# Kernel tuning notes

Hardware: AMD Instinct MI355X
Metric: run time of the kernel (lower is better)

## Reference

```python
import jax, jax.numpy as jnp
import numpy as np

EPS = 1e-08
NEG_WEIGHT = 0.5
B, D = 4096, 256


def setup_inputs() -> dict:
    key = jax.random.key(0)
    k1, k2 = jax.random.split(key)
    feature_a = jax.random.normal(k1, (B, D), dtype=jnp.float32)
    feature_b = jax.random.normal(k2, (B, D), dtype=jnp.float32)
    labels = jnp.ones((B,), dtype=jnp.float32)  # positive pairs on the diagonal block
    return {"feature_a": feature_a, "feature_b": feature_b, "labels": labels}


def reference(feature_a, feature_b, labels):
    b = feature_a.shape[0]
    num_neg = b - 1
    # Cosine via single GEMM instead of the torch repeat/cat loop.
    # torch.nn.CosineSimilarity: dot / max(||a||*||b||, eps)
    na = jnp.sqrt(jnp.sum(feature_a * feature_a, axis=1))  # [B]
    nb = jnp.sqrt(jnp.sum(feature_b * feature_b, axis=1))  # [B]
    dots = jnp.einsum('kd,jd->kj', feature_a, feature_b)   # [B,B] dots[k,j]=a_k.b_j
    # torch ordering: block s (shift), row k pairs a_k with b_{(k+s) % B}
    k = jnp.arange(b)
    s = jnp.arange(b)
    idx = (k[None, :] + s[:, None]) % b                    # [S,K]
    cos = dots[k[None, :], idx] / jnp.maximum(na[None, :] * nb[idx], EPS)  # [S,K]
    logits = ((cos + 1.0) * 0.5).reshape(-1)               # flatten s-major (matches torch cat order)
    labels_full = jnp.concatenate(
        [labels.reshape(-1), jnp.zeros((num_neg * b,), dtype=labels.dtype)])
    weight = jnp.concatenate(
        [jnp.ones((b,), dtype=logits.dtype),
         jnp.full((num_neg * b,), NEG_WEIGHT, dtype=logits.dtype)])
    # BCELoss(weight, reduction='sum') with torch's log clamp at -100
    log_p = jnp.maximum(jnp.log(logits), -100.0)
    log_1mp = jnp.maximum(jnp.log1p(-logits), -100.0)
    loss = -jnp.sum(weight * (labels_full * log_p + (1.0 - labels_full) * log_1mp))
    return (logits, loss)
```

## Files before the change

### kernel.cpp

```cpp
#include <hip/hip_runtime.h>
#include <stdint.h>

#define NB 4096
#define ND 256

typedef __attribute__((ext_vector_type(8))) short short8;
typedef __attribute__((ext_vector_type(4))) float f32x4;

__device__ __forceinline__ unsigned short f2bf(float f) {
    unsigned int u = __float_as_uint(f);
    u += 0x7FFFu + ((u >> 16) & 1u);
    return (unsigned short)(u >> 16);
}

__device__ __forceinline__ void gload16(const void* g, void* lds_uniform) {
    __builtin_amdgcn_global_load_lds(
        (const __attribute__((address_space(1))) void*)(uintptr_t)g,
        (__attribute__((address_space(3))) void*)(unsigned int)(uintptr_t)lds_uniform,
        16, 0, 0);
}

__global__ void __launch_bounds__(256) prep_kernel(
    const float* __restrict__ A, const float* __restrict__ Bf,
    unsigned short* __restrict__ Abf, unsigned short* __restrict__ Bbf,
    float* __restrict__ lossws)
{
    if (blockIdx.x == 0 && threadIdx.x < 64) lossws[threadIdx.x << 5] = 0.0f;
    int gw   = (blockIdx.x * 256 + threadIdx.x) >> 6;
    int lane = threadIdx.x & 63;
    const float* src; unsigned short* dst; int row;
    if (gw < NB) { src = A;  dst = Abf; row = gw; }
    else         { src = Bf; dst = Bbf; row = gw - NB; }

    float4 v = reinterpret_cast<const float4*>(src + (size_t)row * ND)[lane];
    float ss = v.x * v.x + v.y * v.y + v.z * v.z + v.w * v.w;
    #pragma unroll
    for (int off = 1; off < 64; off <<= 1) ss += __shfl_xor(ss, off);
    float rn = 1.0f / sqrtf(fmaxf(ss, 1e-30f));

    ushort4 u;
    u.x = f2bf(v.x * rn); u.y = f2bf(v.y * rn);
    u.z = f2bf(v.z * rn); u.w = f2bf(v.w * rn);
    reinterpret_cast<ushort4*>(dst + (size_t)row * ND)[lane] = u;
}

__global__ void __launch_bounds__(256, 4) gemm_kernel(
    const unsigned short* __restrict__ Abf, const unsigned short* __restrict__ Bbf,
    const float* __restrict__ labels, float* __restrict__ out,
    float* __restrict__ lossws)
{
    __shared__ __align__(16) char smem[40960];

    const int tid = threadIdx.x;
    const int w = tid >> 6, lane = tid & 63;
    const int lane15 = lane & 15, lhi = lane >> 4;
    const int bk = blockIdx.x & 31, bs = blockIdx.x >> 5;
    const int k0 = bk << 7, s0 = bs << 6;
    const int j0 = (k0 + s0) & (NB - 1);

    f32x4 acc[2][5];
    #pragma unroll
    for (int m = 0; m < 2; ++m)
        #pragma unroll
        for (int r = 0; r < 5; ++r) acc[m][r] = (f32x4)0.0f;

    auto stage = [&](int kt, char* buf) {
        #pragma unroll
        for (int i = 0; i < 2; ++i) {
            int slot0 = (i << 8) + (w << 6);
            int slot  = slot0 + lane;
            int row   = slot >> 2;
            int sch   = (slot ^ (slot >> 2) ^ (slot >> 4)) & 3;
            gload16(Abf + (size_t)(k0 + row) * ND + (kt << 5) + (sch << 3), buf + slot0 * 16);
        }
        #pragma unroll
        for (int i = 0; i < 3; ++i) {
            int slot0 = (i << 8) + (w << 6);
            int slot  = slot0 + lane;
            int row   = slot >> 2;
            int srow  = (j0 + row) & (NB - 1);
            int sch   = (slot ^ (slot >> 2) ^ (slot >> 4)) & 3;
            gload16(Bbf + (size_t)srow * ND + (kt << 5) + (sch << 3), buf + 8192 + slot0 * 16);
        }
    };

    stage(0, smem);
    __syncthreads();

    for (int kt = 0; kt < 8; ++kt) {
        char* buf = smem + ((kt & 1) ? 20480 : 0);
        if (kt < 7) stage(kt + 1, smem + ((kt & 1) ? 0 : 20480));
        const int f = (lane15 ^ (lane15 >> 2)) & 3;
        short8 a[2], b[6];
        #pragma unroll
        for (int m = 0; m < 2; ++m) {
            int row = (w << 5) + (m << 4) + lane15;
            a[m] = *reinterpret_cast<const short8*>(buf + row * 64 + ((lhi ^ f) << 4));
        }
        #pragma unroll
        for (int jf = 0; jf < 6; ++jf) {
            int row = (w << 5) + (jf << 4) + lane15;
            b[jf] = *reinterpret_cast<const short8*>(buf + 8192 + row * 64 + ((lhi ^ f) << 4));
        }
        #pragma unroll
        for (int m = 0; m < 2; ++m)
            #pragma unroll
            for (int r = 0; r < 5; ++r)
                acc[m][r] = __builtin_amdgcn_mfma_f32_16x16x32_bf16(
                    a[m], b[m + r], acc[m][r], 0, 0, 0);
        __syncthreads();
    }

    float* dw    = reinterpret_cast<float*>(smem);
    float* lpart = reinterpret_cast<float*>(smem + 32768);
    #pragma unroll
    for (int m = 0; m < 2; ++m)
        #pragma unroll
        for (int r = 0; r < 5; ++r)
            #pragma unroll
            for (int e = 0; e < 4; ++e) {
                int t = (r << 4) + lane15 - (lhi << 2) - e;
                if ((unsigned)t < 64u) {
                    int kap = (w << 5) + (m << 4) + (lhi << 2) + e;
                    dw[(t << 7) + (kap ^ (t & 31))] = acc[m][r][e];
                }
            }
    __syncthreads();

    const int t = w + (lane15 << 2);
    const int s = s0 + t;
    const int x3 = w & 3;
    const float* rowp = dw + (t << 7);
    float lacc = 0.0f;

    #pragma unroll
    for (int i = 0; i < 8; ++i) {
        int qlog  = lhi + (i << 2);
        int physq = qlog ^ (lane15 & 7);
        f32x4 d = *reinterpret_cast<const f32x4*>(rowp + (physq << 2));
        f32x4 v;
        if      (x3 == 0) { v = d; }
        else if (x3 == 1) { v[0] = d[1]; v[1] = d[0]; v[2] = d[3]; v[3] = d[2]; }
        else if (x3 == 2) { v[0] = d[2]; v[1] = d[3]; v[2] = d[0]; v[3] = d[1]; }
        else              { v[0] = d[3]; v[1] = d[2]; v[2] = d[1]; v[3] = d[0]; }

        f32x4 x, y;
        #pragma unroll
        for (int e = 0; e < 4; ++e) {
            x[e] = fmaf(v[e],  0.5f, 0.5f);
            y[e] = fmaf(v[e], -0.5f, 0.5f);
        }
        *reinterpret_cast<f32x4*>(out + (size_t)s * NB + k0 + (qlog << 2)) = x;

        float l1p0 = fmaxf(__logf(y[0]), -100.0f);
        float l1p1 = fmaxf(__logf(y[1]), -100.0f);
        float l1p2 = fmaxf(__logf(y[2]), -100.0f);
        float l1p3 = fmaxf(__logf(y[3]), -100.0f);
        if (s == 0) {
            float l1pv[4] = {l1p0, l1p1, l1p2, l1p3};
            #pragma unroll
            for (int e = 0; e < 4; ++e) {
                float lab = labels[k0 + (qlog << 2) + e];
                float lp  = fmaxf(__logf(x[e]), -100.0f);
                lacc += lab * lp + (1.0f - lab) * l1pv[e];
            }
        } else {
            lacc += 0.5f * (l1p0 + l1p1 + l1p2 + l1p3);
        }
    }

    #pragma unroll
    for (int off = 32; off > 0; off >>= 1) lacc += __shfl_down(lacc, off);
    if (lane == 0) lpart[w] = lacc;
    __syncthreads();
    if (tid == 0) {
        float tot = lpart[0] + lpart[1] + lpart[2] + lpart[3];
        atomicAdd(lossws + ((blockIdx.x & 63) << 5), -tot);
    }
}

__global__ void finalize_kernel(const float* __restrict__ lossws, float* __restrict__ out) {
    float s = 0.0f;
    for (int i = 0; i < 64; ++i) s += lossws[i << 5];
    out[(size_t)NB * NB] = s;
}

extern "C" void kernel_launch(void* const* d_in, const int* in_sizes, int n_in,
                              void* d_out, int out_size, void* d_ws, size_t ws_size,
                              hipStream_t stream) {
    (void)in_sizes; (void)n_in; (void)out_size; (void)ws_size;
    const float* A      = (const float*)d_in[0];
    const float* Bf     = (const float*)d_in[1];
    const float* labels = (const float*)d_in[2];
    float* out = (float*)d_out;

    char* ws = (char*)d_ws;
    unsigned short* Abf = (unsigned short*)ws;
    unsigned short* Bbf = (unsigned short*)(ws + (size_t)2 * 1024 * 1024);
    float* lossws = (float*)(ws + (size_t)4 * 1024 * 1024);

    hipLaunchKernelGGL(prep_kernel, dim3(2048), dim3(256), 0, stream,
                       A, Bf, Abf, Bbf, lossws);
    hipLaunchKernelGGL(gemm_kernel, dim3(2048), dim3(256), 0, stream,
                       Abf, Bbf, labels, out, lossws);
    hipLaunchKernelGGL(finalize_kernel, dim3(1), dim3(1), 0, stream, lossws, out);
}
```

Baseline: 47.33 us.

## Fold finalize into GEMM via completion counter; use explicit vmcnt waits

Drops the separate single-thread finalize kernel. The last GEMM block to finish, detected with an atomic completion counter that prep_kernel resets, sums the loss partials and writes the loss. The K-loop replaces __syncthreads with explicit s_waitcnt vmcnt plus raw s_barrier and sched barriers, so the next stage's loads stay in flight while the current tile is consumed. This removes one kernel launch and the full waits on outstanding loads, but it depends on hand-counted vmcnt values being correct for the async LDS loads.

```diff
diff --git a/kernel.cpp b/kernel.cpp
--- a/kernel.cpp
+++ b/kernel.cpp
@@ -23,9 +23,12 @@
 __global__ void __launch_bounds__(256) prep_kernel(
     const float* __restrict__ A, const float* __restrict__ Bf,
     unsigned short* __restrict__ Abf, unsigned short* __restrict__ Bbf,
-    float* __restrict__ lossws)
+    float* __restrict__ lossws, unsigned int* __restrict__ donecnt)
 {
-    if (blockIdx.x == 0 && threadIdx.x < 64) lossws[threadIdx.x << 5] = 0.0f;
+    if (blockIdx.x == 0) {
+        if (threadIdx.x < 64) lossws[threadIdx.x << 5] = 0.0f;
+        if (threadIdx.x == 64) *donecnt = 0u;
+    }
     int gw   = (blockIdx.x * 256 + threadIdx.x) >> 6;
     int lane = threadIdx.x & 63;
     const float* src; unsigned short* dst; int row;
@@ -47,7 +50,7 @@
 __global__ void __launch_bounds__(256, 4) gemm_kernel(
     const unsigned short* __restrict__ Abf, const unsigned short* __restrict__ Bbf,
     const float* __restrict__ labels, float* __restrict__ out,
-    float* __restrict__ lossws)
+    float* __restrict__ lossws, unsigned int* __restrict__ donecnt)
 {
     __shared__ __align__(16) char smem[40960];
 
@@ -85,11 +88,20 @@
     };
 
     stage(0, smem);
-    __syncthreads();
-
+
+    #pragma unroll
     for (int kt = 0; kt < 8; ++kt) {
         char* buf = smem + ((kt & 1) ? 20480 : 0);
-        if (kt < 7) stage(kt + 1, smem + ((kt & 1) ? 0 : 20480));
+        if (kt < 7) {
+            stage(kt + 1, smem + ((kt & 1) ? 0 : 20480));
+            asm volatile("s_waitcnt vmcnt(5)" ::: "memory");
+        } else {
+            asm volatile("s_waitcnt vmcnt(0)" ::: "memory");
+        }
+        __builtin_amdgcn_sched_barrier(0);
+        __builtin_amdgcn_s_barrier();
+        __builtin_amdgcn_sched_barrier(0);
+
         const int f = (lane15 ^ (lane15 >> 2)) & 3;
         short8 a[2], b[6];
         #pragma unroll
@@ -108,7 +120,10 @@
             for (int r = 0; r < 5; ++r)
                 acc[m][r] = __builtin_amdgcn_mfma_f32_16x16x32_bf16(
                     a[m], b[m + r], acc[m][r], 0, 0, 0);
-        __syncthreads();
+
+        __builtin_amdgcn_sched_barrier(0);
+        __builtin_amdgcn_s_barrier();
+        __builtin_amdgcn_sched_barrier(0);
     }
 
     float* dw    = reinterpret_cast<float*>(smem);
@@ -176,13 +191,16 @@
     if (tid == 0) {
         float tot = lpart[0] + lpart[1] + lpart[2] + lpart[3];
         atomicAdd(lossws + ((blockIdx.x & 63) << 5), -tot);
-    }
-}
-
-__global__ void finalize_kernel(const float* __restrict__ lossws, float* __restrict__ out) {
-    float s = 0.0f;
-    for (int i = 0; i < 64; ++i) s += lossws[i << 5];
-    out[(size_t)NB * NB] = s;
+        __threadfence();
+        unsigned int old = atomicAdd(donecnt, 1u);
+        if (old == 2047u) {
+            __threadfence();
+            float ssum = 0.0f;
+            for (int i = 0; i < 64; ++i)
+                ssum += atomicAdd(lossws + (i << 5), 0.0f);
+            out[(size_t)NB * NB] = ssum;
+        }
+    }
 }
 
 extern "C" void kernel_launch(void* const* d_in, const int* in_sizes, int n_in,
@@ -198,10 +216,10 @@
     unsigned short* Abf = (unsigned short*)ws;
     unsigned short* Bbf = (unsigned short*)(ws + (size_t)2 * 1024 * 1024);
     float* lossws = (float*)(ws + (size_t)4 * 1024 * 1024);
+    unsigned int* donecnt = (unsigned int*)(ws + (size_t)4 * 1024 * 1024 + 8192);
 
     hipLaunchKernelGGL(prep_kernel, dim3(2048), dim3(256), 0, stream,
-                       A, Bf, Abf, Bbf, lossws);
+                       A, Bf, Abf, Bbf, lossws, donecnt);
     hipLaunchKernelGGL(gemm_kernel, dim3(2048), dim3(256), 0, stream,
-                       Abf, Bbf, labels, out, lossws);
-    hipLaunchKernelGGL(finalize_kernel, dim3(1), dim3(1), 0, stream, lossws, out);
-}
+                       Abf, Bbf, labels, out, lossws, donecnt);
+}
```

Measured after the change: 129.8 us. 174% more time.
